# Optimization experiments

Measured on AMD Instinct MI355X. Metric: run time of the kernel, lower is better.

Reference implementation:

```python
import jax, jax.numpy as jnp
import numpy as np

M_POS = 0.5
M_NEG_SIM = 0.1
LAM_NEG = 1.0


def setup_inputs() -> dict:
    key = jax.random.key(0)
    N, d, G = 8192, 1024, 64
    codebook = jax.random.normal(key, (N, d), dtype=jnp.float32)
    base = (jnp.arange(N) // G) * G  # contiguous groups of size G (vq_to_range)
    starts = base.astype(jnp.int32)
    ends = (base + G - 1).astype(jnp.int32)
    return {"codebook": codebook, "starts": starts, "ends": ends, "max_i": N - 1}


def reference(codebook, starts, ends, max_i):
    N, d = codebook.shape
    M = min(N, int(max_i) + 1)  # rows processed by the python loop

    # cosine similarity rows [0:M] vs all N
    zn = codebook / jnp.linalg.norm(codebook, axis=-1, keepdims=True)
    cos = jnp.einsum('md,nd->mn', zn[:M], zn)  # (M, N)

    # pairwise Euclidean distances rows [0:M] vs all N via ||a-b||^2 = |a|^2+|b|^2-2ab
    sq = jnp.sum(codebook * codebook, axis=-1)  # (N,)
    dot = jnp.einsum('md,nd->mn', codebook[:M], codebook)  # (M, N)
    d2 = jnp.maximum(sq[:M, None] + sq[None, :] - 2.0 * dot, 0.0)

    j = jnp.arange(N)[None, :]
    i = jnp.arange(M)[:, None]
    in_range = (j >= starts[:M, None]) & (j <= ends[:M, None])
    pos_mask = in_range & (j != i)
    # original: group_mask[i]=False then neg = ~group_mask, so i is in negatives
    neg_mask = (~in_range) | (j == i)

    pos_cnt = jnp.sum(pos_mask, axis=-1)
    neg_cnt = jnp.sum(neg_mask, axis=-1)

    # safe sqrt: only evaluate on positive-mask entries
    D = jnp.sqrt(jnp.where(pos_mask, d2, 1.0))
    pos_term = jnp.square(jax.nn.relu(D - M_POS)) * pos_mask
    pos_pull = jnp.sum(pos_term, axis=-1) / jnp.maximum(pos_cnt, 1)

    neg_cos = jnp.clip(cos, -1.0, 1.0)
    neg_term = jnp.square(jax.nn.relu(jnp.abs(neg_cos) - M_NEG_SIM)) * neg_mask
    ortho = jnp.sum(neg_term, axis=-1) / jnp.maximum(neg_cnt, 1)

    valid = (pos_cnt > 0) & (neg_cnt > 0)
    per_row = jnp.where(valid, pos_pull + LAM_NEG * ortho, 0.0)
    cnt = jnp.sum(valid)
    total = jnp.sum(per_row)
    return jnp.where(cnt > 0, total / jnp.maximum(cnt, 1).astype(total.dtype), jnp.zeros((), total.dtype))
```

## Files before the change

### kernel.cpp

```cpp
#include <hip/hip_runtime.h>
#include <hip/hip_bf16.h>
#include <stdint.h>

#define M_POS 0.5f
#define M_NEG 0.1f
#define LAM_NEG 1.0f

typedef __attribute__((ext_vector_type(4))) float floatx4;
typedef __attribute__((ext_vector_type(8))) int   intx8;

union Frag8 { intx8 v; int4 q[2]; };

__global__ __launch_bounds__(256) void prep_kernel(
    const float* __restrict__ cb, unsigned char* __restrict__ cb_q,
    float* __restrict__ sq, float* __restrict__ inv_norm,
    unsigned* __restrict__ zero_base, int zero_len,
    int N, int d)
{
    const int gi = blockIdx.x * 256 + threadIdx.x;
    if (gi < zero_len) zero_base[gi] = 0u;

    const int row = blockIdx.x;
    const float* src = cb + (size_t)row * d;
    unsigned char* dst = cb_q + (size_t)row * d;
    const int t = threadIdx.x;

    float s = 0.f;
    for (int c = t * 4; c < d; c += 1024) {
        float4 v = *(const float4*)(src + c);
        s += v.x * v.x + v.y * v.y + v.z * v.z + v.w * v.w;
        int pk = __builtin_amdgcn_cvt_pk_fp8_f32(v.x, v.y, 0, false);
        pk     = __builtin_amdgcn_cvt_pk_fp8_f32(v.z, v.w, pk, true);
        *(int*)(dst + c) = pk;
    }
    for (int o = 32; o > 0; o >>= 1) s += __shfl_down(s, o, 64);
    __shared__ float wsum[4];
    if ((t & 63) == 0) wsum[t >> 6] = s;
    __syncthreads();
    if (t == 0) {
        float tot = wsum[0] + wsum[1] + wsum[2] + wsum[3];
        sq[row] = tot;
        inv_norm[row] = rsqrtf(tot);
    }
}

__global__ __launch_bounds__(256, 3) void gram_loss_kernel(
    const unsigned char* __restrict__ A,
    const float* __restrict__ sq, const float* __restrict__ inv_norm,
    const int* __restrict__ starts, const int* __restrict__ ends,
    const int* __restrict__ max_ip,
    float* __restrict__ pos_acc, float* __restrict__ neg_acc,
    unsigned* __restrict__ counter, float* __restrict__ out,
    int N, int d)
{
    const int M = min(N, max_ip[0] + 1);

    int vt = blockIdx.x;
    const int nB = gridDim.x;
    if ((nB & 7) == 0) {
        const int per = nB >> 3;
        vt = (blockIdx.x & 7) * per + (blockIdx.x >> 3);
    }

    int bx = (int)((sqrtf(8.f * (float)vt + 1.f) - 1.f) * 0.5f);
    while ((bx + 1) * (bx + 2) / 2 <= vt) bx++;
    while (bx * (bx + 1) / 2 > vt) bx--;
    const int by = vt - bx * (bx + 1) / 2;

    const int rowBase = by * 128;
    const int colBase = bx * 128;
    const bool isDiag = (by == bx);

    __shared__ alignas(16) unsigned char ldsA[128 * 128];
    __shared__ alignas(16) unsigned char ldsB[128 * 128];

    const int tid  = threadIdx.x;
    const int wave = tid >> 6;
    const int lane = tid & 63;
    const int wr = (wave >> 1) * 64;
    const int wc = (wave & 1) * 64;

    floatx4 acc[4][4];
#pragma unroll
    for (int a = 0; a < 4; ++a)
#pragma unroll
        for (int b = 0; b < 4; ++b) acc[a][b] = (floatx4){0.f, 0.f, 0.f, 0.f};

    const int sRow = lane >> 3;
    const int sChk = lane & 7;
    const int srcOffC = ((sChk ^ sRow) * 16);
    const int kTiles = d / 128;

    const int rl = lane & 15;
    const int g  = lane >> 4;
    const int rx = rl & 7;
    const int c0 = (((2 * g)     ^ rx) * 16);
    const int c1 = (((2 * g + 1) ^ rx) * 16);

    for (int kt = 0; kt < kTiles; ++kt) {
        __syncthreads();
        const int k0 = kt * 128;
#pragma unroll
        for (int h = 0; h < 4; ++h) {
            const int r = wave * 32 + h * 8 + sRow;
            const unsigned char* ga = A + (size_t)(rowBase + r) * d + k0 + srcOffC;
            const unsigned char* gb = A + (size_t)(colBase + r) * d + k0 + srcOffC;
            __builtin_amdgcn_global_load_lds(
                (const __attribute__((address_space(1))) void*)ga,
                (__attribute__((address_space(3))) void*)(ldsA + r * 128 + sChk * 16), 16, 0, 0);
            __builtin_amdgcn_global_load_lds(
                (const __attribute__((address_space(1))) void*)gb,
                (__attribute__((address_space(3))) void*)(ldsB + r * 128 + sChk * 16), 16, 0, 0);
        }
        __syncthreads();

        Frag8 af[4], bf[4];
#pragma unroll
        for (int t4 = 0; t4 < 4; ++t4) {
            const unsigned char* pa = ldsA + (wr + t4 * 16 + rl) * 128;
            af[t4].q[0] = *(const int4*)(pa + c0);
            af[t4].q[1] = *(const int4*)(pa + c1);
            const unsigned char* pb = ldsB + (wc + t4 * 16 + rl) * 128;
            bf[t4].q[0] = *(const int4*)(pb + c0);
            bf[t4].q[1] = *(const int4*)(pb + c1);
        }
#pragma unroll
        for (int rt = 0; rt < 4; ++rt)
#pragma unroll
            for (int ct = 0; ct < 4; ++ct)
                acc[rt][ct] = __builtin_amdgcn_mfma_scale_f32_16x16x128_f8f6f4(
                    af[rt].v, bf[ct].v, acc[rt][ct], 0, 0, 0, 127, 0, 127);
    }

    const int q  = lane >> 4;
    const int jlo = colBase + wc;
    const int ilo = rowBase + wr;

    int   jn[4];
    float jinv[4];
    bool  jvalid[4];
#pragma unroll
    for (int ct = 0; ct < 4; ++ct) {
        const int j = jlo + ct * 16 + rl;
        jn[ct]  = j;
        jinv[ct] = inv_norm[j];
        jvalid[ct] = (j < M);
    }

    bool posLane = false;
    {
        const int ri = ilo + lane;
        if (ri < M) posLane |= (ends[ri] >= jlo) && (starts[ri] <= jlo + 63);
        if (!isDiag) {
            const int cj = jlo + lane;
            if (cj < M) posLane |= (ends[cj] >= ilo) && (starts[cj] <= ilo + 63);
        }
    }
    const bool fullPath = (__ballot(posLane) != 0ULL);

    float posc[4] = {0.f, 0.f, 0.f, 0.f};
    float negc[4] = {0.f, 0.f, 0.f, 0.f};

    if (fullPath) {
        int   jns[4], jne[4];
        float jsq[4];
#pragma unroll
        for (int ct = 0; ct < 4; ++ct) {
            jsq[ct] = sq[jn[ct]];
            jns[ct] = jvalid[ct] ? starts[jn[ct]] : 0;
            jne[ct] = jvalid[ct] ? ends[jn[ct]]   : -1;
        }
#pragma unroll
        for (int rt = 0; rt < 4; ++rt) {
            const int ibase = ilo + rt * 16 + q * 4;
#pragma unroll
            for (int reg = 0; reg < 4; ++reg) {
                const int i = ibase + reg;
                const bool rowValid = (i < M);
                const int ns = rowValid ? starts[i] : 0;
                const int ne = rowValid ? ends[i]   : -1;
                const float iinv = inv_norm[i];
                const float isq  = sq[i];
                float posp = 0.f, negp = 0.f;
#pragma unroll
                for (int ct = 0; ct < 4; ++ct) {
                    const float dot = acc[rt][ct][reg];
                    const int j = jn[ct];
                    float cosv = dot * iinv * jinv[ct];
                    cosv = fminf(fmaxf(cosv, -1.f), 1.f);
                    float tn = fmaxf(fabsf(cosv) - M_NEG, 0.f);
                    const float nterm = tn * tn;
                    const float d2 = fmaxf(isq + jsq[ct] - 2.f * dot, 0.f);
                    float tp = fmaxf(sqrtf(d2) - M_POS, 0.f);
                    const float pterm = tp * tp;
                    const bool dg = (j == i);
                    if (rowValid) {
                        const bool in_r = (j >= ns) && (j <= ne);
                        if (in_r && !dg) posp += pterm;
                        if (!in_r || dg) negp += nterm;
                    }
                    if (!isDiag && jvalid[ct]) {
                        const bool in_c = (i >= jns[ct]) && (i <= jne[ct]);
                        if (in_c && !dg) posc[ct] += pterm;
                        if (!in_c || dg) negc[ct] += nterm;
                    }
                }
#pragma unroll
                for (int m = 1; m < 16; m <<= 1) {
                    posp += __shfl_xor(posp, m, 64);
                    negp += __shfl_xor(negp, m, 64);
                }
                if (rowValid && rl == 0) {
                    atomicAdd(&pos_acc[i], posp);
                    atomicAdd(&neg_acc[i], negp);
                }
            }
        }
        if (!isDiag) {
#pragma unroll
            for (int ct = 0; ct < 4; ++ct) {
                posc[ct] += __shfl_xor(posc[ct], 16, 64);
                posc[ct] += __shfl_xor(posc[ct], 32, 64);
                negc[ct] += __shfl_xor(negc[ct], 16, 64);
                negc[ct] += __shfl_xor(negc[ct], 32, 64);
            }
            if (q == 0) {
#pragma unroll
                for (int ct = 0; ct < 4; ++ct) {
                    if (jvalid[ct]) {
                        atomicAdd(&pos_acc[jn[ct]], posc[ct]);
                        atomicAdd(&neg_acc[jn[ct]], negc[ct]);
                    }
                }
            }
        }
    } else {
#pragma unroll
        for (int rt = 0; rt < 4; ++rt) {
            const int ibase = ilo + rt * 16 + q * 4;
#pragma unroll
            for (int reg = 0; reg < 4; ++reg) {
                const int i = ibase + reg;
                const float iinv = inv_norm[i];
                float negp = 0.f;
#pragma unroll
                for (int ct = 0; ct < 4; ++ct) {
                    const float dot = acc[rt][ct][reg];
                    float cosv = dot * iinv * jinv[ct];
                    cosv = fminf(fmaxf(cosv, -1.f), 1.f);
                    float tn = fmaxf(fabsf(cosv) - M_NEG, 0.f);
                    const float nterm = tn * tn;
                    negp += nterm;
                    negc[ct] += nterm;
                }
#pragma unroll
                for (int m = 1; m < 16; m <<= 1)
                    negp += __shfl_xor(negp, m, 64);
                if ((i < M) && rl == 0)
                    atomicAdd(&neg_acc[i], negp);
            }
        }
        if (!isDiag) {
#pragma unroll
            for (int ct = 0; ct < 4; ++ct) {
                negc[ct] += __shfl_xor(negc[ct], 16, 64);
                negc[ct] += __shfl_xor(negc[ct], 32, 64);
            }
            if (q == 0) {
#pragma unroll
                for (int ct = 0; ct < 4; ++ct)
                    if (jvalid[ct])
                        atomicAdd(&neg_acc[jn[ct]], negc[ct]);
            }
        }
    }

    __shared__ bool amLast;
    __syncthreads();
    if (tid == 0) {
        __threadfence();
        unsigned old = atomicAdd(counter, 1u);
        amLast = (old == (unsigned)(gridDim.x - 1));
    }
    __syncthreads();
    if (amLast) {
        __threadfence();
        float total = 0.f;
        int cnt = 0;
        for (int i = tid; i < M; i += 256) {
            const float pa = __hip_atomic_load(&pos_acc[i], __ATOMIC_RELAXED, __HIP_MEMORY_SCOPE_AGENT);
            const float na = __hip_atomic_load(&neg_acc[i], __ATOMIC_RELAXED, __HIP_MEMORY_SCOPE_AGENT);
            const int ns = starts[i], ne = ends[i];
            const int lo = max(ns, 0), hi = min(ne, N - 1);
            const int inr = max(hi - lo + 1, 0);
            const bool dg = (i >= ns) && (i <= ne);
            const int pos_cnt = inr - (dg ? 1 : 0);
            const int neg_cnt = N - inr + (dg ? 1 : 0);
            if (pos_cnt > 0 && neg_cnt > 0) {
                total += pa / (float)max(pos_cnt, 1)
                       + LAM_NEG * na / (float)max(neg_cnt, 1);
                cnt++;
            }
        }
        for (int o = 32; o > 0; o >>= 1) {
            total += __shfl_down(total, o, 64);
            cnt   += __shfl_down(cnt, o, 64);
        }
        __shared__ float fin_ts[4];
        __shared__ int   fin_cs[4];
        if ((tid & 63) == 0) { fin_ts[tid >> 6] = total; fin_cs[tid >> 6] = cnt; }
        __syncthreads();
        if (tid == 0) {
            float T = fin_ts[0] + fin_ts[1] + fin_ts[2] + fin_ts[3];
            int   C = fin_cs[0] + fin_cs[1] + fin_cs[2] + fin_cs[3];
            out[0] = (C > 0) ? T / (float)C : 0.f;
        }
    }
}

extern "C" void kernel_launch(void* const* d_in, const int* in_sizes, int n_in,
                              void* d_out, int out_size, void* d_ws, size_t ws_size,
                              hipStream_t stream) {
    const float* cb     = (const float*)d_in[0];
    const int*   starts = (const int*)d_in[1];
    const int*   ends   = (const int*)d_in[2];
    const int*   max_ip = (const int*)d_in[3];
    float* out = (float*)d_out;

    const int N = in_sizes[1];
    const int d = in_sizes[0] / N;

    char* ws = (char*)d_ws;
    unsigned char* cb_q = (unsigned char*)ws;
    size_t off = ((size_t)N * d + 255) & ~(size_t)255;
    float* sq       = (float*)(ws + off); off += (size_t)N * 4;
    float* inv_norm = (float*)(ws + off); off += (size_t)N * 4;
    float* pos_acc  = (float*)(ws + off); off += (size_t)N * 4;
    float* neg_acc  = (float*)(ws + off); off += (size_t)N * 4;
    unsigned* counter = (unsigned*)(ws + off); off += 256;

    prep_kernel<<<N, 256, 0, stream>>>(cb, cb_q, sq, inv_norm,
                                       (unsigned*)pos_acc, 2 * N + 1, N, d);

    const int nb = N / 128;
    const int nBlocks = nb * (nb + 1) / 2;
    gram_loss_kernel<<<nBlocks, 256, 0, stream>>>(cb_q, sq, inv_norm, starts, ends,
                                                  max_ip, pos_acc, neg_acc, counter,
                                                  out, N, d);
}
```

Measured before the change: 199.7 us.

## Load MFMA fragments directly from global memory with register double buffering

Removes the LDS staging and the block-level barriers from the fp8 Gram-matrix main loop. Each wave now loads its A/B fragments straight from global memory into registers, using two register buffers so the next k-tile's loads overlap the current tile's MFMAs. This doubles fragment register use, so launch bounds drop from 3 to 2 blocks per CU. The trade-off is lost cross-wave data sharing through LDS: each row is now fetched redundantly by two waves, which adds global/L2 traffic.

```diff
diff --git a/kernel.cpp b/kernel.cpp
--- a/kernel.cpp
+++ b/kernel.cpp
@@ -44,7 +44,7 @@
     }
 }
 
-__global__ __launch_bounds__(256, 3) void gram_loss_kernel(
+__global__ __launch_bounds__(256, 2) void gram_loss_kernel(
     const unsigned char* __restrict__ A,
     const float* __restrict__ sq, const float* __restrict__ inv_norm,
     const int* __restrict__ starts, const int* __restrict__ ends,
@@ -71,9 +71,6 @@
     const int colBase = bx * 128;
     const bool isDiag = (by == bx);
 
-    __shared__ alignas(16) unsigned char ldsA[128 * 128];
-    __shared__ alignas(16) unsigned char ldsB[128 * 128];
-
     const int tid  = threadIdx.x;
     const int wave = tid >> 6;
     const int lane = tid & 63;
@@ -86,51 +83,48 @@
 #pragma unroll
         for (int b = 0; b < 4; ++b) acc[a][b] = (floatx4){0.f, 0.f, 0.f, 0.f};
 
-    const int sRow = lane >> 3;
-    const int sChk = lane & 7;
-    const int srcOffC = ((sChk ^ sRow) * 16);
-    const int kTiles = d / 128;
-
     const int rl = lane & 15;
     const int g  = lane >> 4;
-    const int rx = rl & 7;
-    const int c0 = (((2 * g)     ^ rx) * 16);
-    const int c1 = (((2 * g + 1) ^ rx) * 16);
-
-    for (int kt = 0; kt < kTiles; ++kt) {
-        __syncthreads();
-        const int k0 = kt * 128;
-#pragma unroll
-        for (int h = 0; h < 4; ++h) {
-            const int r = wave * 32 + h * 8 + sRow;
-            const unsigned char* ga = A + (size_t)(rowBase + r) * d + k0 + srcOffC;
-            const unsigned char* gb = A + (size_t)(colBase + r) * d + k0 + srcOffC;
-            __builtin_amdgcn_global_load_lds(
-                (const __attribute__((address_space(1))) void*)ga,
-                (__attribute__((address_space(3))) void*)(ldsA + r * 128 + sChk * 16), 16, 0, 0);
-            __builtin_amdgcn_global_load_lds(
-                (const __attribute__((address_space(1))) void*)gb,
-                (__attribute__((address_space(3))) void*)(ldsB + r * 128 + sChk * 16), 16, 0, 0);
-        }
-        __syncthreads();
-
-        Frag8 af[4], bf[4];
-#pragma unroll
-        for (int t4 = 0; t4 < 4; ++t4) {
-            const unsigned char* pa = ldsA + (wr + t4 * 16 + rl) * 128;
-            af[t4].q[0] = *(const int4*)(pa + c0);
-            af[t4].q[1] = *(const int4*)(pa + c1);
-            const unsigned char* pb = ldsB + (wc + t4 * 16 + rl) * 128;
-            bf[t4].q[0] = *(const int4*)(pb + c0);
-            bf[t4].q[1] = *(const int4*)(pb + c1);
-        }
-#pragma unroll
-        for (int rt = 0; rt < 4; ++rt)
-#pragma unroll
-            for (int ct = 0; ct < 4; ++ct)
-                acc[rt][ct] = __builtin_amdgcn_mfma_scale_f32_16x16x128_f8f6f4(
-                    af[rt].v, bf[ct].v, acc[rt][ct], 0, 0, 0, 127, 0, 127);
-    }
+
+    const unsigned char* aRow0 = A + (size_t)(rowBase + wr + rl) * d + g * 32;
+    const unsigned char* bRow0 = A + (size_t)(colBase + wc + rl) * d + g * 32;
+    const size_t rstep = (size_t)16 * d;
+
+    const int kTiles = d / 128;
+
+    Frag8 aX[4], bX[4], aY[4], bY[4];
+
+#define LOADF(AF, BF, KOFF)                                                  \
+    { _Pragma("unroll")                                                      \
+      for (int t4 = 0; t4 < 4; ++t4) {                                       \
+        const unsigned char* pa = aRow0 + (size_t)t4 * rstep + (KOFF);       \
+        const unsigned char* pb = bRow0 + (size_t)t4 * rstep + (KOFF);       \
+        AF[t4].q[0] = *(const int4*)(pa);                                    \
+        AF[t4].q[1] = *(const int4*)(pa + 16);                               \
+        BF[t4].q[0] = *(const int4*)(pb);                                    \
+        BF[t4].q[1] = *(const int4*)(pb + 16);                               \
+      } }
+
+#define MFMAS(AF, BF)                                                        \
+    { _Pragma("unroll")                                                      \
+      for (int rt = 0; rt < 4; ++rt)                                         \
+        _Pragma("unroll")                                                    \
+        for (int ct = 0; ct < 4; ++ct)                                       \
+          acc[rt][ct] = __builtin_amdgcn_mfma_scale_f32_16x16x128_f8f6f4(    \
+              AF[rt].v, BF[ct].v, acc[rt][ct], 0, 0, 0, 127, 0, 127); }
+
+    LOADF(aX, bX, 0)
+    int kt = 0;
+    for (;;) {
+        if (kt + 1 < kTiles) LOADF(aY, bY, (kt + 1) * 128)
+        MFMAS(aX, bX)
+        ++kt; if (kt >= kTiles) break;
+        if (kt + 1 < kTiles) LOADF(aX, bX, (kt + 1) * 128)
+        MFMAS(aY, bY)
+        ++kt; if (kt >= kTiles) break;
+    }
+#undef LOADF
+#undef MFMAS
 
     const int q  = lane >> 4;
     const int jlo = colBase + wc;
```

Measured after the change: 288.4 us. 1.44x slower.

## Double-buffer LDS tiles to prefetch next K-tile during MFMA compute

Applied to the files above, without the earlier changes.

The single LDS A/B tile pair becomes two buffers. The next K-tile is issued with global_load_lds into the idle buffer while MFMAs consume the current one, so the two barriers per iteration become one waitcnt plus barrier. This is meant to hide global-to-LDS latency within a block. The cost is double the LDS per block, and the occupancy hint drops from 3 to 2 blocks per CU, which reduces the latency hiding that came from running more blocks at once.

```diff
diff --git a/kernel.cpp b/kernel.cpp
--- a/kernel.cpp
+++ b/kernel.cpp
@@ -44,7 +44,7 @@
     }
 }
 
-__global__ __launch_bounds__(256, 3) void gram_loss_kernel(
+__global__ __launch_bounds__(256, 2) void gram_loss_kernel(
     const unsigned char* __restrict__ A,
     const float* __restrict__ sq, const float* __restrict__ inv_norm,
     const int* __restrict__ starts, const int* __restrict__ ends,
@@ -71,8 +71,8 @@
     const int colBase = bx * 128;
     const bool isDiag = (by == bx);
 
-    __shared__ alignas(16) unsigned char ldsA[128 * 128];
-    __shared__ alignas(16) unsigned char ldsB[128 * 128];
+    __shared__ alignas(16) unsigned char ldsA[2][128 * 128];
+    __shared__ alignas(16) unsigned char ldsB[2][128 * 128];
 
     const int tid  = threadIdx.x;
     const int wave = tid >> 6;
@@ -97,30 +97,40 @@
     const int c0 = (((2 * g)     ^ rx) * 16);
     const int c1 = (((2 * g + 1) ^ rx) * 16);
 
+#define STAGE(BUF, KT)                                                          \
+    { const int k0_ = (KT) * 128;                                               \
+      _Pragma("unroll")                                                         \
+      for (int h = 0; h < 4; ++h) {                                             \
+        const int r_ = wave * 32 + h * 8 + sRow;                                \
+        const unsigned char* ga_ = A + (size_t)(rowBase + r_) * d + k0_ + srcOffC; \
+        const unsigned char* gb_ = A + (size_t)(colBase + r_) * d + k0_ + srcOffC; \
+        __builtin_amdgcn_global_load_lds(                                       \
+            (const __attribute__((address_space(1))) void*)ga_,                 \
+            (__attribute__((address_space(3))) void*)(ldsA[BUF] + r_ * 128 + sChk * 16), 16, 0, 0); \
+        __builtin_amdgcn_global_load_lds(                                       \
+            (const __attribute__((address_space(1))) void*)gb_,                 \
+            (__attribute__((address_space(3))) void*)(ldsB[BUF] + r_ * 128 + sChk * 16), 16, 0, 0); \
+      } }
+
+    STAGE(0, 0)
+    asm volatile("s_waitcnt vmcnt(0)" ::: "memory");
+    __builtin_amdgcn_s_barrier();
+
+    int cur = 0;
     for (int kt = 0; kt < kTiles; ++kt) {
-        __syncthreads();
-        const int k0 = kt * 128;
-#pragma unroll
-        for (int h = 0; h < 4; ++h) {
-            const int r = wave * 32 + h * 8 + sRow;
-            const unsigned char* ga = A + (size_t)(rowBase + r) * d + k0 + srcOffC;
-            const unsigned char* gb = A + (size_t)(colBase + r) * d + k0 + srcOffC;
-            __builtin_amdgcn_global_load_lds(
-                (const __attribute__((address_space(1))) void*)ga,
-                (__attribute__((address_space(3))) void*)(ldsA + r * 128 + sChk * 16), 16, 0, 0);
-            __builtin_amdgcn_global_load_lds(
-                (const __attribute__((address_space(1))) void*)gb,
-                (__attribute__((address_space(3))) void*)(ldsB + r * 128 + sChk * 16), 16, 0, 0);
-        }
-        __syncthreads();
+        const bool more = (kt + 1 < kTiles);
+        if (more) {
+            if (cur == 0) STAGE(1, kt + 1)
+            else          STAGE(0, kt + 1)
+        }
 
         Frag8 af[4], bf[4];
 #pragma unroll
         for (int t4 = 0; t4 < 4; ++t4) {
-            const unsigned char* pa = ldsA + (wr + t4 * 16 + rl) * 128;
+            const unsigned char* pa = ldsA[cur] + (wr + t4 * 16 + rl) * 128;
             af[t4].q[0] = *(const int4*)(pa + c0);
             af[t4].q[1] = *(const int4*)(pa + c1);
-            const unsigned char* pb = ldsB + (wc + t4 * 16 + rl) * 128;
+            const unsigned char* pb = ldsB[cur] + (wc + t4 * 16 + rl) * 128;
             bf[t4].q[0] = *(const int4*)(pb + c0);
             bf[t4].q[1] = *(const int4*)(pb + c1);
         }
@@ -130,7 +140,14 @@
             for (int ct = 0; ct < 4; ++ct)
                 acc[rt][ct] = __builtin_amdgcn_mfma_scale_f32_16x16x128_f8f6f4(
                     af[rt].v, bf[ct].v, acc[rt][ct], 0, 0, 0, 127, 0, 127);
-    }
+
+        if (more) {
+            asm volatile("s_waitcnt vmcnt(0)" ::: "memory");
+            __builtin_amdgcn_s_barrier();
+            cur ^= 1;
+        }
+    }
+#undef STAGE
 
     const int q  = lane >> 4;
     const int jlo = colBase + wc;
```

Result: slower. 232.2 us (+16.3%).
